# Kernel optimization log

Measured on AMD Instinct MI355X. Metric: run time of the kernel, lower is better.

Reference implementation:

```python
import jax, jax.numpy as jnp
import numpy as np

QMIN, QMAX = -128.0, 127.0  # 8-bit signed activation range


def fq_act(x, s):
    """Fake-quantize activations: clip(round(x/s))*s with straight-through estimator."""
    y = jnp.clip(jnp.round(x / s), QMIN, QMAX) * s
    return x + jax.lax.stop_gradient(y - x)


def fq_weight(w):
    """Per-tensor max-abs symmetric (narrow-range) 8-bit weight fake-quant with STE."""
    s = jnp.max(jnp.abs(w)) / 127.0
    y = jnp.clip(jnp.round(w / s), -127.0, 127.0) * s
    return w + jax.lax.stop_gradient(y - w)


def conv1x1(x, w, b):
    # x: [b,c,h,w], w: [o,c] -> [b,o,h,w]
    return jnp.einsum('bchw,oc->bohw', x, w) + b[None, :, None, None]


def setup_inputs() -> dict:
    key = jax.random.key(0)
    ks = jax.random.split(key, 6)
    B, C, HC, H, W = 8, 64, 32, 64, 64
    x = jax.random.normal(ks[0], (B, C, H, W), dtype=jnp.float32)
    wq = jax.random.normal(ks[1], (HC, C), dtype=jnp.float32) * 0.05
    wk = jax.random.normal(ks[2], (HC, C), dtype=jnp.float32) * 0.05
    wv = jax.random.normal(ks[3], (HC, C), dtype=jnp.float32) * 0.05
    wp = jax.random.normal(ks[4], (C, HC), dtype=jnp.float32) * 0.05
    return {
        'x': x,
        'wq': wq, 'bq': jnp.zeros((HC,), jnp.float32),
        'wk': wk, 'bk': jnp.zeros((HC,), jnp.float32),
        'wv': wv, 'bv': jnp.zeros((HC,), jnp.float32),
        'wp': wp, 'bp': jnp.zeros((C,), jnp.float32),
        's_in': jnp.ones((1,), jnp.float32) * 0.0625,
        's_out': jnp.ones((1,), jnp.float32) * 0.0625,
    }


def reference(x, wq, bq, wk, bk, wv, bv, wp, bp, s_in, s_out):
    b, c, h, w = x.shape
    hc = wq.shape[0]
    n = h * w
    xq = fq_act(x, s_in)                              # quant_inp(x)
    q = conv1x1(xq, fq_weight(wq), bq).reshape(b, hc, n).transpose(0, 2, 1)  # [b,n,hc]
    k = conv1x1(xq, fq_weight(wk), bk).reshape(b, hc, n)                     # [b,hc,n]
    v = conv1x1(xq, fq_weight(wv), bv).reshape(b, hc, n).transpose(0, 2, 1)  # [b,n,hc]
    z = jax.nn.softmax(jnp.einsum('bqc,bck->bqk', q, k), axis=-1)            # [b,n,n]
    z = jnp.einsum('bqk,bkc->bqc', z, v).transpose(0, 2, 1).reshape(b, hc, h, w)
    z = fq_act(z, s_in)                               # quant_inp(z) (shared module/scale)
    out = xq + conv1x1(z, fq_weight(wp), bp)
    return fq_act(out, s_out)                         # self.act QuantIdentity
```

## Files before the change

kernel.cpp:

```cpp
#include <hip/hip_runtime.h>
#include <hip/hip_bf16.h>
#include <cstdint>
#include <cstddef>

#define NB 8
#define NC 64
#define NHC 32
#define NN 4096
#define LOG2E 1.44269504088896340736f

typedef short v8s __attribute__((ext_vector_type(8)));
typedef float v4f __attribute__((ext_vector_type(4)));

__device__ __forceinline__ unsigned short f2b(float f) {
    unsigned int u = __builtin_bit_cast(unsigned int, f);
    u += 0x7fffu + ((u >> 16) & 1u);
    return (unsigned short)(u >> 16);
}
__device__ __forceinline__ float b2f(unsigned short s) {
    unsigned int u = ((unsigned int)s) << 16;
    return __builtin_bit_cast(float, u);
}
__device__ __forceinline__ unsigned int pack2_bf16(float a, float b) {
    unsigned int ua = __builtin_bit_cast(unsigned int, a);
    ua += 0x7fffu + ((ua >> 16) & 1u);
    unsigned int ub = __builtin_bit_cast(unsigned int, b);
    ub += 0x7fffu + ((ub >> 16) & 1u);
    return (ua >> 16) | (ub & 0xffff0000u);
}
__device__ __forceinline__ unsigned int trunc2_bf16(float a, float b) {
    return __builtin_amdgcn_perm(__builtin_bit_cast(unsigned int, b),
                                 __builtin_bit_cast(unsigned int, a), 0x07060302u);
}

__global__ __launch_bounds__(256) void k_qkv(
    const float* __restrict__ x,
    const float* __restrict__ wq, const float* __restrict__ wk, const float* __restrict__ wv,
    const float* __restrict__ bq, const float* __restrict__ bk, const float* __restrict__ bv,
    const float* __restrict__ s_in,
    unsigned short* __restrict__ xqb, unsigned short* __restrict__ qb,
    unsigned short* __restrict__ kb, unsigned short* __restrict__ vb)
{
    int blk = blockIdx.x;
    int b   = blk >> 6;
    int p0  = (blk & 63) * 64;
    int tid = threadIdx.x;

    __shared__ __align__(16) unsigned short xt[64][72];
    __shared__ __align__(16) unsigned short wlds[6144];
    __shared__ float red[3][256];

    float4 q0 = *(const float4*)(wq + tid * 8), q1 = *(const float4*)(wq + tid * 8 + 4);
    float4 k0 = *(const float4*)(wk + tid * 8), k1 = *(const float4*)(wk + tid * 8 + 4);
    float4 v0 = *(const float4*)(wv + tid * 8), v1 = *(const float4*)(wv + tid * 8 + 4);
    float mq = fmaxf(fmaxf(fmaxf(fabsf(q0.x), fabsf(q0.y)), fmaxf(fabsf(q0.z), fabsf(q0.w))),
                     fmaxf(fmaxf(fabsf(q1.x), fabsf(q1.y)), fmaxf(fabsf(q1.z), fabsf(q1.w))));
    float mk = fmaxf(fmaxf(fmaxf(fabsf(k0.x), fabsf(k0.y)), fmaxf(fabsf(k0.z), fabsf(k0.w))),
                     fmaxf(fmaxf(fabsf(k1.x), fabsf(k1.y)), fmaxf(fabsf(k1.z), fabsf(k1.w))));
    float mv = fmaxf(fmaxf(fmaxf(fabsf(v0.x), fabsf(v0.y)), fmaxf(fabsf(v0.z), fabsf(v0.w))),
                     fmaxf(fmaxf(fabsf(v1.x), fabsf(v1.y)), fmaxf(fabsf(v1.z), fabsf(v1.w))));
    red[0][tid] = mq; red[1][tid] = mk; red[2][tid] = mv;
    __syncthreads();
    for (int s = 128; s > 0; s >>= 1) {
        if (tid < s) {
            red[0][tid] = fmaxf(red[0][tid], red[0][tid + s]);
            red[1][tid] = fmaxf(red[1][tid], red[1][tid + s]);
            red[2][tid] = fmaxf(red[2][tid], red[2][tid + s]);
        }
        __syncthreads();
    }
    float sq = red[0][0] / 127.0f, sk = red[1][0] / 127.0f, sw = red[2][0] / 127.0f;
    {
        const float* srcs[3] = {wq, wk, wv};
        float scl[3] = {sq, sk, sw};
        #pragma unroll
        for (int t = 0; t < 3; ++t) {
            #pragma unroll
            for (int j = 0; j < 8; ++j) {
                float val = srcs[t][tid * 8 + j];
                float r = fminf(fmaxf(rintf(val / scl[t]), -127.f), 127.f);
                wlds[t * 2048 + tid * 8 + j] = f2b(r * scl[t]);
            }
        }
    }

    float sv = s_in[0];
    float sinv = 1.0f / sv;
    int jj = tid & 15;
    int c0 = tid >> 4;
    #pragma unroll
    for (int it = 0; it < 4; ++it) {
        int c = c0 + it * 16;
        size_t gi = ((size_t)(b * NC + c) << 12) + p0 + jj * 4;
        float4 xv = *(const float4*)(x + gi);
        float r0 = fminf(fmaxf(rintf(xv.x * sinv), -128.f), 127.f) * sv;
        float r1 = fminf(fmaxf(rintf(xv.y * sinv), -128.f), 127.f) * sv;
        float r2 = fminf(fmaxf(rintf(xv.z * sinv), -128.f), 127.f) * sv;
        float r3 = fminf(fmaxf(rintf(xv.w * sinv), -128.f), 127.f) * sv;
        *(uint2*)(xqb + gi) = make_uint2(pack2_bf16(r0, r1), pack2_bf16(r2, r3));
        xt[jj * 4 + 0][c] = f2b(r0);
        xt[jj * 4 + 1][c] = f2b(r1);
        xt[jj * 4 + 2][c] = f2b(r2);
        xt[jj * 4 + 3][c] = f2b(r3);
    }
    __syncthreads();

    int wave = tid >> 6;
    int lane = tid & 63;
    int quad = lane >> 4;
    int l15  = lane & 15;

    v8s bf0 = *(const v8s*)(&xt[wave * 16 + l15][0  + quad * 8]);
    v8s bf1 = *(const v8s*)(&xt[wave * 16 + l15][32 + quad * 8]);

    int pos = p0 + wave * 16 + l15;
    size_t posg = (size_t)b * NN + pos;
    const v4f zc = {0.f, 0.f, 0.f, 0.f};

    #pragma unroll
    for (int rb = 0; rb < 6; ++rb) {
        v8s a0 = *(const v8s*)(wlds + (rb * 16 + l15) * 64 + 0  + quad * 8);
        v8s a1 = *(const v8s*)(wlds + (rb * 16 + l15) * 64 + 32 + quad * 8);
        v4f t   = __builtin_amdgcn_mfma_f32_16x16x32_bf16(a0, bf0, zc, 0, 0, 0);
        v4f acc = __builtin_amdgcn_mfma_f32_16x16x32_bf16(a1, bf1, t, 0, 0, 0);

        int R0 = rb * 16 + quad * 4;
        float vals[4];
        #pragma unroll
        for (int r = 0; r < 4; ++r) {
            int R = R0 + r;
            float bias = (R < 32) ? bq[R] : (R < 64) ? bk[R - 32] : bv[R - 64];
            float vv = acc[r] + bias;
            if (R < 32) vv *= LOG2E;
            vals[r] = vv;
        }
        if (R0 < 32) {
            *(unsigned int*)(qb + posg * NHC + R0)     = pack2_bf16(vals[0], vals[1]);
            *(unsigned int*)(qb + posg * NHC + R0 + 2) = pack2_bf16(vals[2], vals[3]);
        } else if (R0 < 64) {
            *(unsigned int*)(kb + posg * NHC + R0 - 32)     = pack2_bf16(vals[0], vals[1]);
            *(unsigned int*)(kb + posg * NHC + R0 - 32 + 2) = pack2_bf16(vals[2], vals[3]);
        } else {
            #pragma unroll
            for (int r = 0; r < 4; ++r)
                vb[(size_t)(b * NHC + R0 - 64 + r) * NN + pos] = f2b(vals[r]);
        }
    }
}

__global__ __launch_bounds__(256, 2) void k_attn(
    const unsigned short* __restrict__ qb, const unsigned short* __restrict__ kb,
    const unsigned short* __restrict__ vb, const unsigned short* __restrict__ xqb,
    const float* __restrict__ wp, const float* __restrict__ bp,
    const float* __restrict__ s_in, const float* __restrict__ s_out,
    float* __restrict__ out)
{
    int blk  = blockIdx.x;
    int b    = blk >> 6;
    int qt   = blk & 63;
    int qbase = qt * 64;
    int tid  = threadIdx.x;
    int wave = tid >> 6;
    int lane = tid & 63;
    int quad = lane >> 4;
    int l15  = lane & 15;

    __shared__ __align__(16) unsigned short pbuf[4][16 * 72];
    __shared__ __align__(16) float zbuf[4][64][36];
    __shared__ float lbuf[4][64];
    __shared__ __align__(16) unsigned short wpq[2048];
    __shared__ float red[256];

    {
        float4 a0 = *(const float4*)(wp + tid * 8), a1 = *(const float4*)(wp + tid * 8 + 4);
        float mx = fmaxf(fmaxf(fmaxf(fabsf(a0.x), fabsf(a0.y)), fmaxf(fabsf(a0.z), fabsf(a0.w))),
                         fmaxf(fmaxf(fabsf(a1.x), fabsf(a1.y)), fmaxf(fabsf(a1.z), fabsf(a1.w))));
        red[tid] = mx;
        __syncthreads();
        for (int s = 128; s > 0; s >>= 1) {
            if (tid < s) red[tid] = fmaxf(red[tid], red[tid + s]);
            __syncthreads();
        }
        float scale = red[0] / 127.0f;
        float e[8] = {a0.x, a0.y, a0.z, a0.w, a1.x, a1.y, a1.z, a1.w};
        #pragma unroll
        for (int j = 0; j < 8; ++j) {
            float r = fminf(fmaxf(rintf(e[j] / scale), -127.f), 127.f);
            wpq[tid * 8 + j] = f2b(r * scale);
        }
    }

    unsigned short* pb = pbuf[wave];
    const unsigned short* qbat = qb + (size_t)b * NN * NHC;
    const unsigned short* kbat = kb + (size_t)b * NN * NHC;
    const unsigned short* vbat = vb + (size_t)b * NHC * NN;

    v8s qf[4];
    #pragma unroll
    for (int s = 0; s < 4; ++s)
        qf[s] = *(const v8s*)(qbat + (qbase + s * 16 + l15) * NHC + quad * 8);

    const short one_bf16 = (short)0x3F80;
    const v8s ones = {one_bf16, one_bf16, one_bf16, one_bf16,
                      one_bf16, one_bf16, one_bf16, one_bf16};
    const v4f zc = {0.f, 0.f, 0.f, 0.f};
    v4f zt[4][2] = {{zc, zc}, {zc, zc}, {zc, zc}, {zc, zc}};
    v4f lacc[4] = {zc, zc, zc, zc};

    int k0 = wave * 1024;
    const unsigned short* vrow0 = vbat + (size_t)( 0 + l15) * NN;
    const unsigned short* vrow1 = vbat + (size_t)(16 + l15) * NN;

    v8s ck0 = *(const v8s*)(kbat + (k0 +  0 + l15) * NHC + quad * 8);
    v8s ck1 = *(const v8s*)(kbat + (k0 + 16 + l15) * NHC + quad * 8);
    v8s ck2 = *(const v8s*)(kbat + (k0 + 32 + l15) * NHC + quad * 8);
    v8s ck3 = *(const v8s*)(kbat + (k0 + 48 + l15) * NHC + quad * 8);

    for (int i = 0; i < 16; ++i) {
        int cki = k0 + (i << 6);
        int nki = k0 + (((i + 1) & 15) << 6);
        v8s nk0 = *(const v8s*)(kbat + (nki +  0 + l15) * NHC + quad * 8);
        v8s nk1 = *(const v8s*)(kbat + (nki + 16 + l15) * NHC + quad * 8);
        v8s nk2 = *(const v8s*)(kbat + (nki + 32 + l15) * NHC + quad * 8);
        v8s nk3 = *(const v8s*)(kbat + (nki + 48 + l15) * NHC + quad * 8);
        v8s cv0 = *(const v8s*)(vrow0 + cki +  0 + quad * 8);
        v8s cv1 = *(const v8s*)(vrow0 + cki + 32 + quad * 8);
        v8s cv2 = *(const v8s*)(vrow1 + cki +  0 + quad * 8);
        v8s cv3 = *(const v8s*)(vrow1 + cki + 32 + quad * 8);

        #pragma unroll
        for (int s = 0; s < 4; ++s) {
            v4f sa[4];
            sa[0] = __builtin_amdgcn_mfma_f32_16x16x32_bf16(ck0, qf[s], zc, 0, 0, 0);
            sa[1] = __builtin_amdgcn_mfma_f32_16x16x32_bf16(ck1, qf[s], zc, 0, 0, 0);
            sa[2] = __builtin_amdgcn_mfma_f32_16x16x32_bf16(ck2, qf[s], zc, 0, 0, 0);
            sa[3] = __builtin_amdgcn_mfma_f32_16x16x32_bf16(ck3, qf[s], zc, 0, 0, 0);

            #pragma unroll
            for (int t = 0; t < 4; ++t) {
                float p0 = __builtin_amdgcn_exp2f(sa[t][0]);
                float p1 = __builtin_amdgcn_exp2f(sa[t][1]);
                float p2 = __builtin_amdgcn_exp2f(sa[t][2]);
                float p3 = __builtin_amdgcn_exp2f(sa[t][3]);
                *(uint2*)(pb + l15 * 72 + 16 * t + quad * 4) =
                    make_uint2(trunc2_bf16(p0, p1), trunc2_bf16(p2, p3));
            }
            v8s pf0 = *(const v8s*)(pb + l15 * 72 +  0 + quad * 8);
            v8s pf1 = *(const v8s*)(pb + l15 * 72 + 32 + quad * 8);

            zt[s][0] = __builtin_amdgcn_mfma_f32_16x16x32_bf16(cv0, pf0, zt[s][0], 0, 0, 0);
            zt[s][0] = __builtin_amdgcn_mfma_f32_16x16x32_bf16(cv1, pf1, zt[s][0], 0, 0, 0);
            zt[s][1] = __builtin_amdgcn_mfma_f32_16x16x32_bf16(cv2, pf0, zt[s][1], 0, 0, 0);
            zt[s][1] = __builtin_amdgcn_mfma_f32_16x16x32_bf16(cv3, pf1, zt[s][1], 0, 0, 0);
            lacc[s]  = __builtin_amdgcn_mfma_f32_16x16x32_bf16(ones, pf0, lacc[s], 0, 0, 0);
            lacc[s]  = __builtin_amdgcn_mfma_f32_16x16x32_bf16(ones, pf1, lacc[s], 0, 0, 0);
        }
        ck0 = nk0; ck1 = nk1; ck2 = nk2; ck3 = nk3;
    }

    #pragma unroll
    for (int s = 0; s < 4; ++s) {
        *(v4f*)(&zbuf[wave][s * 16 + l15][     quad * 4]) = zt[s][0];
        *(v4f*)(&zbuf[wave][s * 16 + l15][16 + quad * 4]) = zt[s][1];
        if (quad == 0) lbuf[wave][s * 16 + l15] = lacc[s][0];
    }
    __syncthreads();

    int myq = wave * 16 + l15;
    float L = lbuf[0][myq] + lbuf[1][myq] + lbuf[2][myq] + lbuf[3][myq];

    float z[8] = {0.f};
    #pragma unroll
    for (int w = 0; w < 4; ++w) {
        v4f za  = *(const v4f*)(&zbuf[w][myq][quad * 8]);
        v4f zb2 = *(const v4f*)(&zbuf[w][myq][quad * 8 + 4]);
        #pragma unroll
        for (int j = 0; j < 4; ++j) { z[j] += za[j]; z[4 + j] += zb2[j]; }
    }
    float sv = s_in[0], sinv = 1.0f / sv;
    float so = s_out[0], soinv = 1.0f / so;
    float Linv = 1.0f / L;
    unsigned int zp[4];
    #pragma unroll
    for (int jp = 0; jp < 4; ++jp) {
        float a = z[2 * jp]     * Linv;
        float c = z[2 * jp + 1] * Linv;
        a = fminf(fmaxf(rintf(a * sinv), -128.f), 127.f) * sv;
        c = fminf(fmaxf(rintf(c * sinv), -128.f), 127.f) * sv;
        zp[jp] = pack2_bf16(a, c);
    }
    v8s zf = __builtin_bit_cast(v8s, *(uint4*)zp);

    v8s w0f = *(const v8s*)(wpq + ( 0 + l15) * NHC + quad * 8);
    v8s w1f = *(const v8s*)(wpq + (16 + l15) * NHC + quad * 8);
    v8s w2f = *(const v8s*)(wpq + (32 + l15) * NHC + quad * 8);
    v8s w3f = *(const v8s*)(wpq + (48 + l15) * NHC + quad * 8);
    v4f o0 = __builtin_amdgcn_mfma_f32_16x16x32_bf16(w0f, zf, zc, 0, 0, 0);
    v4f o1 = __builtin_amdgcn_mfma_f32_16x16x32_bf16(w1f, zf, zc, 0, 0, 0);
    v4f o2 = __builtin_amdgcn_mfma_f32_16x16x32_bf16(w2f, zf, zc, 0, 0, 0);
    v4f o3 = __builtin_amdgcn_mfma_f32_16x16x32_bf16(w3f, zf, zc, 0, 0, 0);

    int pos = qbase + wave * 16 + l15;
    #pragma unroll
    for (int ot = 0; ot < 4; ++ot) {
        v4f ov = (ot == 0) ? o0 : (ot == 1) ? o1 : (ot == 2) ? o2 : o3;
        #pragma unroll
        for (int r = 0; r < 4; ++r) {
            int oc = ot * 16 + quad * 4 + r;
            size_t idx = (size_t)(b * NC + oc) * NN + pos;
            float val = ov[r] + bp[oc] + b2f(xqb[idx]);
            float f = fminf(fmaxf(rintf(val * soinv), -128.f), 127.f);
            out[idx] = f * so;
        }
    }
}

extern "C" void kernel_launch(void* const* d_in, const int* in_sizes, int n_in,
                              void* d_out, int out_size, void* d_ws, size_t ws_size,
                              hipStream_t stream) {
    const float* x     = (const float*)d_in[0];
    const float* wq    = (const float*)d_in[1];
    const float* bq    = (const float*)d_in[2];
    const float* wk    = (const float*)d_in[3];
    const float* bk    = (const float*)d_in[4];
    const float* wv    = (const float*)d_in[5];
    const float* bv    = (const float*)d_in[6];
    const float* wp    = (const float*)d_in[7];
    const float* bp    = (const float*)d_in[8];
    const float* s_in  = (const float*)d_in[9];
    const float* s_out = (const float*)d_in[10];
    float* out = (float*)d_out;

    char* ws = (char*)d_ws;
    size_t off = 0;
    auto carve = [&](size_t bytes) {
        void* p = ws + off;
        off = (off + bytes + 255) & ~(size_t)255;
        return p;
    };
    unsigned short* xqb = (unsigned short*)carve((size_t)NB * NC * NN * 2);
    unsigned short* qbf = (unsigned short*)carve((size_t)NB * NN * NHC * 2);
    unsigned short* kbf = (unsigned short*)carve((size_t)NB * NN * NHC * 2);
    unsigned short* vbf = (unsigned short*)carve((size_t)NB * NHC * NN * 2);

    hipLaunchKernelGGL(k_qkv, dim3(512), dim3(256), 0, stream,
                       x, wq, wk, wv, bq, bk, bv, s_in, xqb, qbf, kbf, vbf);
    hipLaunchKernelGGL(k_attn, dim3(512), dim3(256), 0, stream,
                       qbf, kbf, vbf, xqb, wp, bp, s_in, s_out, out);
}
```

Before: 118.4 us.

## Batch score MFMAs across slices, use wave-shuffle reductions, double QKV tile size

In the attention loop, the P buffer becomes one slot per query slice, so the score MFMAs for two slices are issued together before their exp2 and P stores. All P·V MFMAs then run afterwards, which gives more independent MFMA work between LDS round trips. The weight max-abs reductions replace the LDS tree and its barrier chain with wave shuffles. The QKV kernel handles 128 positions per block with half as many blocks, so the weight quantization is amortized over more positions. The cost is higher LDS use (pbuf grows fourfold) and more register pressure, which could reduce occupancy in the attention kernel.

New measurement: 120.2 us. No clear change (+1.5%).

```diff
diff --git a/kernel.cpp b/kernel.cpp
--- a/kernel.cpp
+++ b/kernel.cpp
@@ -31,6 +31,11 @@
 __device__ __forceinline__ unsigned int trunc2_bf16(float a, float b) {
     return __builtin_amdgcn_perm(__builtin_bit_cast(unsigned int, b),
                                  __builtin_bit_cast(unsigned int, a), 0x07060302u);
+}
+__device__ __forceinline__ float wave_max(float v) {
+    #pragma unroll
+    for (int off = 1; off < 64; off <<= 1) v = fmaxf(v, __shfl_xor(v, off));
+    return v;
 }
 
 __global__ __launch_bounds__(256) void k_qkv(
@@ -42,13 +47,15 @@
     unsigned short* __restrict__ kb, unsigned short* __restrict__ vb)
 {
     int blk = blockIdx.x;
-    int b   = blk >> 6;
-    int p0  = (blk & 63) * 64;
+    int b   = blk >> 5;
+    int p0  = (blk & 31) * 128;
     int tid = threadIdx.x;
-
-    __shared__ __align__(16) unsigned short xt[64][72];
+    int wave = tid >> 6;
+    int lane = tid & 63;
+
+    __shared__ __align__(16) unsigned short xt[128][72];
     __shared__ __align__(16) unsigned short wlds[6144];
-    __shared__ float red[3][256];
+    __shared__ float red[3][4];
 
     float4 q0 = *(const float4*)(wq + tid * 8), q1 = *(const float4*)(wq + tid * 8 + 4);
     float4 k0 = *(const float4*)(wk + tid * 8), k1 = *(const float4*)(wk + tid * 8 + 4);
@@ -59,38 +66,31 @@
                      fmaxf(fmaxf(fabsf(k1.x), fabsf(k1.y)), fmaxf(fabsf(k1.z), fabsf(k1.w))));
     float mv = fmaxf(fmaxf(fmaxf(fabsf(v0.x), fabsf(v0.y)), fmaxf(fabsf(v0.z), fabsf(v0.w))),
                      fmaxf(fmaxf(fabsf(v1.x), fabsf(v1.y)), fmaxf(fabsf(v1.z), fabsf(v1.w))));
-    red[0][tid] = mq; red[1][tid] = mk; red[2][tid] = mv;
+    mq = wave_max(mq); mk = wave_max(mk); mv = wave_max(mv);
+    if (lane == 0) { red[0][wave] = mq; red[1][wave] = mk; red[2][wave] = mv; }
     __syncthreads();
-    for (int s = 128; s > 0; s >>= 1) {
-        if (tid < s) {
-            red[0][tid] = fmaxf(red[0][tid], red[0][tid + s]);
-            red[1][tid] = fmaxf(red[1][tid], red[1][tid + s]);
-            red[2][tid] = fmaxf(red[2][tid], red[2][tid + s]);
-        }
-        __syncthreads();
-    }
-    float sq = red[0][0] / 127.0f, sk = red[1][0] / 127.0f, sw = red[2][0] / 127.0f;
+    float sq = fmaxf(fmaxf(red[0][0], red[0][1]), fmaxf(red[0][2], red[0][3])) / 127.0f;
+    float sk = fmaxf(fmaxf(red[1][0], red[1][1]), fmaxf(red[1][2], red[1][3])) / 127.0f;
+    float sw = fmaxf(fmaxf(red[2][0], red[2][1]), fmaxf(red[2][2], red[2][3])) / 127.0f;
     {
-        const float* srcs[3] = {wq, wk, wv};
-        float scl[3] = {sq, sk, sw};
-        #pragma unroll
-        for (int t = 0; t < 3; ++t) {
-            #pragma unroll
-            for (int j = 0; j < 8; ++j) {
-                float val = srcs[t][tid * 8 + j];
-                float r = fminf(fmaxf(rintf(val / scl[t]), -127.f), 127.f);
-                wlds[t * 2048 + tid * 8 + j] = f2b(r * scl[t]);
-            }
+        float eq[8] = {q0.x, q0.y, q0.z, q0.w, q1.x, q1.y, q1.z, q1.w};
+        float ek[8] = {k0.x, k0.y, k0.z, k0.w, k1.x, k1.y, k1.z, k1.w};
+        float ev[8] = {v0.x, v0.y, v0.z, v0.w, v1.x, v1.y, v1.z, v1.w};
+        #pragma unroll
+        for (int j = 0; j < 8; ++j) {
+            wlds[0 * 2048 + tid * 8 + j] = f2b(fminf(fmaxf(rintf(eq[j] / sq), -127.f), 127.f) * sq);
+            wlds[1 * 2048 + tid * 8 + j] = f2b(fminf(fmaxf(rintf(ek[j] / sk), -127.f), 127.f) * sk);
+            wlds[2 * 2048 + tid * 8 + j] = f2b(fminf(fmaxf(rintf(ev[j] / sw), -127.f), 127.f) * sw);
         }
     }
 
     float sv = s_in[0];
     float sinv = 1.0f / sv;
-    int jj = tid & 15;
-    int c0 = tid >> 4;
-    #pragma unroll
-    for (int it = 0; it < 4; ++it) {
-        int c = c0 + it * 16;
+    int jj = tid & 31;
+    int c0 = tid >> 5;
+    #pragma unroll
+    for (int it = 0; it < 8; ++it) {
+        int c = c0 + it * 8;
         size_t gi = ((size_t)(b * NC + c) << 12) + p0 + jj * 4;
         float4 xv = *(const float4*)(x + gi);
         float r0 = fminf(fmaxf(rintf(xv.x * sinv), -128.f), 127.f) * sv;
@@ -105,45 +105,46 @@
     }
     __syncthreads();
 
-    int wave = tid >> 6;
-    int lane = tid & 63;
     int quad = lane >> 4;
     int l15  = lane & 15;
-
-    v8s bf0 = *(const v8s*)(&xt[wave * 16 + l15][0  + quad * 8]);
-    v8s bf1 = *(const v8s*)(&xt[wave * 16 + l15][32 + quad * 8]);
-
-    int pos = p0 + wave * 16 + l15;
-    size_t posg = (size_t)b * NN + pos;
     const v4f zc = {0.f, 0.f, 0.f, 0.f};
 
     #pragma unroll
-    for (int rb = 0; rb < 6; ++rb) {
-        v8s a0 = *(const v8s*)(wlds + (rb * 16 + l15) * 64 + 0  + quad * 8);
-        v8s a1 = *(const v8s*)(wlds + (rb * 16 + l15) * 64 + 32 + quad * 8);
-        v4f t   = __builtin_amdgcn_mfma_f32_16x16x32_bf16(a0, bf0, zc, 0, 0, 0);
-        v4f acc = __builtin_amdgcn_mfma_f32_16x16x32_bf16(a1, bf1, t, 0, 0, 0);
-
-        int R0 = rb * 16 + quad * 4;
-        float vals[4];
-        #pragma unroll
-        for (int r = 0; r < 4; ++r) {
-            int R = R0 + r;
-            float bias = (R < 32) ? bq[R] : (R < 64) ? bk[R - 32] : bv[R - 64];
-            float vv = acc[r] + bias;
-            if (R < 32) vv *= LOG2E;
-            vals[r] = vv;
-        }
-        if (R0 < 32) {
-            *(unsigned int*)(qb + posg * NHC + R0)     = pack2_bf16(vals[0], vals[1]);
-            *(unsigned int*)(qb + posg * NHC + R0 + 2) = pack2_bf16(vals[2], vals[3]);
-        } else if (R0 < 64) {
-            *(unsigned int*)(kb + posg * NHC + R0 - 32)     = pack2_bf16(vals[0], vals[1]);
-            *(unsigned int*)(kb + posg * NHC + R0 - 32 + 2) = pack2_bf16(vals[2], vals[3]);
-        } else {
+    for (int sub = 0; sub < 2; ++sub) {
+        int prow = wave * 32 + sub * 16 + l15;
+        v8s bf0 = *(const v8s*)(&xt[prow][0  + quad * 8]);
+        v8s bf1 = *(const v8s*)(&xt[prow][32 + quad * 8]);
+        int pos = p0 + wave * 32 + sub * 16 + l15;
+        size_t posg = (size_t)b * NN + pos;
+
+        #pragma unroll
+        for (int rb = 0; rb < 6; ++rb) {
+            v8s a0 = *(const v8s*)(wlds + (rb * 16 + l15) * 64 + 0  + quad * 8);
+            v8s a1 = *(const v8s*)(wlds + (rb * 16 + l15) * 64 + 32 + quad * 8);
+            v4f t   = __builtin_amdgcn_mfma_f32_16x16x32_bf16(a0, bf0, zc, 0, 0, 0);
+            v4f acc = __builtin_amdgcn_mfma_f32_16x16x32_bf16(a1, bf1, t, 0, 0, 0);
+
+            int R0 = rb * 16 + quad * 4;
+            float vals[4];
             #pragma unroll
-            for (int r = 0; r < 4; ++r)
-                vb[(size_t)(b * NHC + R0 - 64 + r) * NN + pos] = f2b(vals[r]);
+            for (int r = 0; r < 4; ++r) {
+                int R = R0 + r;
+                float bias = (R < 32) ? bq[R] : (R < 64) ? bk[R - 32] : bv[R - 64];
+                float vv = acc[r] + bias;
+                if (R < 32) vv *= LOG2E;
+                vals[r] = vv;
+            }
+            if (R0 < 32) {
+                *(unsigned int*)(qb + posg * NHC + R0)     = pack2_bf16(vals[0], vals[1]);
+                *(unsigned int*)(qb + posg * NHC + R0 + 2) = pack2_bf16(vals[2], vals[3]);
+            } else if (R0 < 64) {
+                *(unsigned int*)(kb + posg * NHC + R0 - 32)     = pack2_bf16(vals[0], vals[1]);
+                *(unsigned int*)(kb + posg * NHC + R0 - 32 + 2) = pack2_bf16(vals[2], vals[3]);
+            } else {
+                #pragma unroll
+                for (int r = 0; r < 4; ++r)
+                    vb[(size_t)(b * NHC + R0 - 64 + r) * NN + pos] = f2b(vals[r]);
+            }
         }
     }
 }
@@ -165,23 +166,20 @@
     int quad = lane >> 4;
     int l15  = lane & 15;
 
-    __shared__ __align__(16) unsigned short pbuf[4][16 * 72];
+    __shared__ __align__(16) unsigned short pbuf[4][4][16 * 72];
     __shared__ __align__(16) float zbuf[4][64][36];
     __shared__ float lbuf[4][64];
     __shared__ __align__(16) unsigned short wpq[2048];
-    __shared__ float red[256];
+    __shared__ float redw[4];
 
     {
         float4 a0 = *(const float4*)(wp + tid * 8), a1 = *(const float4*)(wp + tid * 8 + 4);
         float mx = fmaxf(fmaxf(fmaxf(fabsf(a0.x), fabsf(a0.y)), fmaxf(fabsf(a0.z), fabsf(a0.w))),
                          fmaxf(fmaxf(fabsf(a1.x), fabsf(a1.y)), fmaxf(fabsf(a1.z), fabsf(a1.w))));
-        red[tid] = mx;
+        mx = wave_max(mx);
+        if (lane == 0) redw[wave] = mx;
         __syncthreads();
-        for (int s = 128; s > 0; s >>= 1) {
-            if (tid < s) red[tid] = fmaxf(red[tid], red[tid + s]);
-            __syncthreads();
-        }
-        float scale = red[0] / 127.0f;
+        float scale = fmaxf(fmaxf(redw[0], redw[1]), fmaxf(redw[2], redw[3])) / 127.0f;
         float e[8] = {a0.x, a0.y, a0.z, a0.w, a1.x, a1.y, a1.z, a1.w};
         #pragma unroll
         for (int j = 0; j < 8; ++j) {
@@ -190,7 +188,6 @@
         }
     }
 
-    unsigned short* pb = pbuf[wave];
     const unsigned short* qbat = qb + (size_t)b * NN * NHC;
     const unsigned short* kbat = kb + (size_t)b * NN * NHC;
     const unsigned short* vbat = vb + (size_t)b * NHC * NN;
@@ -229,25 +226,35 @@
         v8s cv3 = *(const v8s*)(vrow1 + cki + 32 + quad * 8);
 
         #pragma unroll
+        for (int g = 0; g < 2; ++g) {
+            v4f sa[2][4];
+            #pragma unroll
+            for (int sl = 0; sl < 2; ++sl) {
+                int s = g * 2 + sl;
+                sa[sl][0] = __builtin_amdgcn_mfma_f32_16x16x32_bf16(ck0, qf[s], zc, 0, 0, 0);
+                sa[sl][1] = __builtin_amdgcn_mfma_f32_16x16x32_bf16(ck1, qf[s], zc, 0, 0, 0);
+                sa[sl][2] = __builtin_amdgcn_mfma_f32_16x16x32_bf16(ck2, qf[s], zc, 0, 0, 0);
+                sa[sl][3] = __builtin_amdgcn_mfma_f32_16x16x32_bf16(ck3, qf[s], zc, 0, 0, 0);
+            }
+            #pragma unroll
+            for (int sl = 0; sl < 2; ++sl) {
+                unsigned short* pb = pbuf[wave][g * 2 + sl];
+                #pragma unroll
+                for (int t = 0; t < 4; ++t) {
+                    float p0 = __builtin_amdgcn_exp2f(sa[sl][t][0]);
+                    float p1 = __builtin_amdgcn_exp2f(sa[sl][t][1]);
+                    float p2 = __builtin_amdgcn_exp2f(sa[sl][t][2]);
+                    float p3 = __builtin_amdgcn_exp2f(sa[sl][t][3]);
+                    *(uint2*)(pb + l15 * 72 + 16 * t + quad * 4) =
+                        make_uint2(trunc2_bf16(p0, p1), trunc2_bf16(p2, p3));
+                }
+            }
+        }
+        #pragma unroll
         for (int s = 0; s < 4; ++s) {
-            v4f sa[4];
-            sa[0] = __builtin_amdgcn_mfma_f32_16x16x32_bf16(ck0, qf[s], zc, 0, 0, 0);
-            sa[1] = __builtin_amdgcn_mfma_f32_16x16x32_bf16(ck1, qf[s], zc, 0, 0, 0);
-            sa[2] = __builtin_amdgcn_mfma_f32_16x16x32_bf16(ck2, qf[s], zc, 0, 0, 0);
-            sa[3] = __builtin_amdgcn_mfma_f32_16x16x32_bf16(ck3, qf[s], zc, 0, 0, 0);
-
-            #pragma unroll
-            for (int t = 0; t < 4; ++t) {
-                float p0 = __builtin_amdgcn_exp2f(sa[t][0]);
-                float p1 = __builtin_amdgcn_exp2f(sa[t][1]);
-                float p2 = __builtin_amdgcn_exp2f(sa[t][2]);
-                float p3 = __builtin_amdgcn_exp2f(sa[t][3]);
-                *(uint2*)(pb + l15 * 72 + 16 * t + quad * 4) =
-                    make_uint2(trunc2_bf16(p0, p1), trunc2_bf16(p2, p3));
-            }
+            const unsigned short* pb = pbuf[wave][s];
             v8s pf0 = *(const v8s*)(pb + l15 * 72 +  0 + quad * 8);
             v8s pf1 = *(const v8s*)(pb + l15 * 72 + 32 + quad * 8);
-
             zt[s][0] = __builtin_amdgcn_mfma_f32_16x16x32_bf16(cv0, pf0, zt[s][0], 0, 0, 0);
             zt[s][0] = __builtin_amdgcn_mfma_f32_16x16x32_bf16(cv1, pf1, zt[s][0], 0, 0, 0);
             zt[s][1] = __builtin_amdgcn_mfma_f32_16x16x32_bf16(cv2, pf0, zt[s][1], 0, 0, 0);
@@ -343,7 +350,7 @@
     unsigned short* kbf = (unsigned short*)carve((size_t)NB * NN * NHC * 2);
     unsigned short* vbf = (unsigned short*)carve((size_t)NB * NHC * NN * 2);
 
-    hipLaunchKernelGGL(k_qkv, dim3(512), dim3(256), 0, stream,
+    hipLaunchKernelGGL(k_qkv, dim3(256), dim3(256), 0, stream,
                        x, wq, wk, wv, bq, bk, bv, s_in, xqb, qbf, kbf, vbf);
     hipLaunchKernelGGL(k_attn, dim3(512), dim3(256), 0, stream,
                        qbf, kbf, vbf, xqb, wp, bp, s_in, s_out, out);
```
